# Optimization experiments

Hardware: AMD Instinct MI355X
Metric: run time of the kernel (lower is better)

Reference implementation:

```python
import jax, jax.numpy as jnp
import numpy as np

B, L, R, E, H = 256, 196, 1024, 1024, 512  # batch, regions, rnn_size, input_encoding, att_hid


def _lstm_cell(x, h, c, Wih, Whh, bih, bhh):
    # PyTorch LSTMCell gate order: i, f, g, o
    gates = x @ Wih.T + bih + h @ Whh.T + bhh  # [B, 4R]
    i, f, g, o = jnp.split(gates, 4, axis=1)
    i, f, o = jax.nn.sigmoid(i), jax.nn.sigmoid(f), jax.nn.sigmoid(o)
    g = jnp.tanh(g)
    c_new = f * c + i * g
    h_new = o * jnp.tanh(c_new)
    return h_new, c_new


def _attention(h, att_feats, p_att, mask, Wh, bh, Wa, ba):
    att_h = h @ Wh.T + bh                       # [B, H]
    dot = jnp.tanh(p_att + att_h[:, None, :])   # [B, L, H]
    scores = jnp.einsum('blh,h->bl', dot, Wa) + ba  # [B, L]
    w = jax.nn.softmax(scores, axis=1)
    w = w * mask
    w = w / (jnp.sum(w, axis=1, keepdims=True) + 1e-10)
    return jnp.einsum('bl,bld->bd', w, att_feats)  # [B, R]


def setup_inputs() -> dict:
    key = jax.random.key(0)
    ks = jax.random.split(key, 32)
    s = 0.05
    inp = {
        'xt': jax.random.normal(ks[0], (B, E), jnp.float32),
        'fc_feats': jax.random.normal(ks[1], (B, 3 * R), jnp.float32),
        'att_feats': jax.random.normal(ks[2], (B, L, R), jnp.float32),
        'p_att_feats': jax.random.normal(ks[3], (B, L, H), jnp.float32),
        'att_masks': jnp.ones((B, L), jnp.float32),
        'att_feats1': jax.random.normal(ks[4], (B, L, R), jnp.float32),
        'p_att_feats1': jax.random.normal(ks[5], (B, L, H), jnp.float32),
        'att_masks1': jnp.ones((B, L), jnp.float32),
        'state_h': jax.random.normal(ks[6], (3, B, R), jnp.float32),
        'state_c': jax.random.normal(ks[7], (3, B, R), jnp.float32),
        # att_lstm0 / att_lstm: input dim E + 2R; lang_lstm: 3R
        'Wih0': jax.random.normal(ks[8], (4 * R, E + 2 * R), jnp.float32) * s,
        'Whh0': jax.random.normal(ks[9], (4 * R, R), jnp.float32) * s,
        'bih0': jnp.zeros((4 * R,), jnp.float32),
        'bhh0': jnp.zeros((4 * R,), jnp.float32),
        'Wih1': jax.random.normal(ks[10], (4 * R, E + 2 * R), jnp.float32) * s,
        'Whh1': jax.random.normal(ks[11], (4 * R, R), jnp.float32) * s,
        'bih1': jnp.zeros((4 * R,), jnp.float32),
        'bhh1': jnp.zeros((4 * R,), jnp.float32),
        'WihL': jax.random.normal(ks[12], (4 * R, 3 * R), jnp.float32) * s,
        'WhhL': jax.random.normal(ks[13], (4 * R, R), jnp.float32) * s,
        'bihL': jnp.zeros((4 * R,), jnp.float32),
        'bhhL': jnp.zeros((4 * R,), jnp.float32),
        # attention0 / attention / attention1 params (h2att + alpha_net)
        'a0_Wh': jax.random.normal(ks[14], (H, R), jnp.float32) * s,
        'a0_bh': jnp.zeros((H,), jnp.float32),
        'a0_Wa': jax.random.normal(ks[15], (H,), jnp.float32) * s,
        'a0_ba': jnp.zeros((), jnp.float32),
        'a_Wh': jax.random.normal(ks[16], (H, R), jnp.float32) * s,
        'a_bh': jnp.zeros((H,), jnp.float32),
        'a_Wa': jax.random.normal(ks[17], (H,), jnp.float32) * s,
        'a_ba': jnp.zeros((), jnp.float32),
        'a1_Wh': jax.random.normal(ks[18], (H, R), jnp.float32) * s,
        'a1_bh': jnp.zeros((H,), jnp.float32),
        'a1_Wa': jax.random.normal(ks[19], (H,), jnp.float32) * s,
        'a1_ba': jnp.zeros((), jnp.float32),
    }
    return inp


def reference(xt, fc_feats, att_feats, p_att_feats, att_masks,
              att_feats1, p_att_feats1, att_masks1, state_h, state_c,
              Wih0, Whh0, bih0, bhh0, Wih1, Whh1, bih1, bhh1,
              WihL, WhhL, bihL, bhhL,
              a0_Wh, a0_bh, a0_Wa, a0_ba,
              a_Wh, a_bh, a_Wa, a_ba,
              a1_Wh, a1_bh, a1_Wa, a1_ba):
    prev_h = state_h[-1]                       # h_lang from previous step
    fc_ori = fc_feats[:, :R]                   # only the first slice is used

    # layer 0: att_lstm0 + attention0 over (att_feats1, p_att_feats1)
    x0 = jnp.concatenate([prev_h, fc_ori, xt], axis=1)
    h_att0, c_att0 = _lstm_cell(x0, state_h[0], state_c[0], Wih0, Whh0, bih0, bhh0)
    att0 = _attention(h_att0, att_feats1, p_att_feats1, att_masks1, a0_Wh, a0_bh, a0_Wa, a0_ba)

    # layer 1: att_lstm + two attentions
    x1 = jnp.concatenate([prev_h, att0, xt], axis=1)
    h_att, c_att = _lstm_cell(x1, state_h[1], state_c[1], Wih1, Whh1, bih1, bhh1)
    att = _attention(h_att, att_feats, p_att_feats, att_masks, a_Wh, a_bh, a_Wa, a_ba)
    att1 = _attention(h_att, att_feats1, p_att_feats1, att_masks1, a1_Wh, a1_bh, a1_Wa, a1_ba)

    # layer 2: lang_lstm
    xL = jnp.concatenate([att, att1, h_att], axis=1)
    h_lang, c_lang = _lstm_cell(xL, state_h[2], state_c[2], WihL, WhhL, bihL, bhhL)

    output = h_lang  # dropout is identity in eval mode
    new_h = jnp.stack([h_att0, h_att, h_lang])
    new_c = jnp.stack([c_att0, c_att, c_lang])
    return output, new_h, new_c
```

## Files before the change

kernel.cpp:

```cpp
#include <hip/hip_runtime.h>
#include <math.h>

#define B_   256
#define L_   196
#define R_   1024
#define E_   1024
#define H_   512
#define G4R  4096
#define DIN  3072

__device__ __forceinline__ float sigmoidf_(float x) {
    return 1.0f / (1.0f + __expf(-x));
}
__device__ __forceinline__ float tanhf_(float x) {
    float ax = fabsf(x);
    float t  = __expf(-2.0f * ax);
    float r  = (1.0f - t) / (1.0f + t);
    return copysignf(r, x);
}

__global__ __launch_bounds__(256) void gemm2_bias(
    const float* __restrict__ A1, const float* __restrict__ W1, int K1,
    const float* __restrict__ A2, const float* __restrict__ W2, int K2,
    const float* __restrict__ bias1, const float* __restrict__ bias2,
    float* __restrict__ C, int N)
{
    __shared__ float As[16][64];
    __shared__ float Ws[16][64];
    const int t  = threadIdx.x;
    const int tx = t & 15, ty = t >> 4;
    const int mBase = blockIdx.x * 64;
    const int nBase = blockIdx.y * 64;
    const int lr = t >> 2;
    const int lk = (t & 3) * 4;

    float acc[4][4];
#pragma unroll
    for (int i = 0; i < 4; i++)
#pragma unroll
        for (int j = 0; j < 4; j++) acc[i][j] = 0.0f;

    for (int seg = 0; seg < 2; ++seg) {
        const int K = seg ? K2 : K1;
        if (K == 0) continue;
        const float* A = seg ? A2 : A1;
        const float* W = seg ? W2 : W1;
        const float* aPtr = A + (size_t)(mBase + lr) * K + lk;
        const float* wPtr = W + (size_t)(nBase + lr) * K + lk;

        float4 av = *(const float4*)(aPtr);
        float4 wv = *(const float4*)(wPtr);

        for (int k0 = 0; k0 < K; k0 += 16) {
            float4 avn, wvn;
            if (k0 + 16 < K) {
                avn = *(const float4*)(aPtr + k0 + 16);
                wvn = *(const float4*)(wPtr + k0 + 16);
            } else { avn = av; wvn = wv; }

            __syncthreads();
            As[lk + 0][lr] = av.x; As[lk + 1][lr] = av.y;
            As[lk + 2][lr] = av.z; As[lk + 3][lr] = av.w;
            Ws[lk + 0][lr] = wv.x; Ws[lk + 1][lr] = wv.y;
            Ws[lk + 2][lr] = wv.z; Ws[lk + 3][lr] = wv.w;
            __syncthreads();

#pragma unroll
            for (int k = 0; k < 16; k++) {
                float4 a = *(const float4*)&As[k][ty * 4];
                float4 b = *(const float4*)&Ws[k][tx * 4];
                acc[0][0] += a.x * b.x; acc[0][1] += a.x * b.y;
                acc[0][2] += a.x * b.z; acc[0][3] += a.x * b.w;
                acc[1][0] += a.y * b.x; acc[1][1] += a.y * b.y;
                acc[1][2] += a.y * b.z; acc[1][3] += a.y * b.w;
                acc[2][0] += a.z * b.x; acc[2][1] += a.z * b.y;
                acc[2][2] += a.z * b.z; acc[2][3] += a.z * b.w;
                acc[3][0] += a.w * b.x; acc[3][1] += a.w * b.y;
                acc[3][2] += a.w * b.z; acc[3][3] += a.w * b.w;
            }
            av = avn; wv = wvn;
        }
    }

#pragma unroll
    for (int i = 0; i < 4; i++) {
        int m = mBase + ty * 4 + i;
#pragma unroll
        for (int j = 0; j < 4; j++) {
            int n = nBase + tx * 4 + j;
            float v = acc[i][j] + bias1[n];
            if (bias2) v += bias2[n];
            C[(size_t)m * N + n] = v;
        }
    }
}

__global__ __launch_bounds__(256) void lstm_cell(
    const float* __restrict__ gates, const float* __restrict__ c_in,
    float* __restrict__ h_out, float* __restrict__ c_out,
    float* __restrict__ h_out2)
{
    int e = blockIdx.x * 256 + threadIdx.x;
    int b = e >> 10;
    int j = e & 1023;
    const float* g = gates + (size_t)b * G4R;
    float i_ = sigmoidf_(g[j]);
    float f_ = sigmoidf_(g[j + 1024]);
    float gg = tanhf_(g[j + 2048]);
    float o_ = sigmoidf_(g[j + 3072]);
    float c  = f_ * c_in[e] + i_ * gg;
    float h  = o_ * tanhf_(c);
    c_out[e] = c;
    h_out[e] = h;
    if (h_out2) h_out2[e] = h;
}

__global__ __launch_bounds__(256) void concat3_1024(
    float* __restrict__ dst,
    const float* __restrict__ s0, int ld0,
    const float* __restrict__ s1, int ld1,
    const float* __restrict__ s2, int ld2)
{
    int e = blockIdx.x * 256 + threadIdx.x;
    int b = e / 3072;
    int c = e - b * 3072;
    int which = c >> 10, off = c & 1023;
    const float* s = (which == 0) ? s0 : (which == 1) ? s1 : s2;
    int ld = (which == 0) ? ld0 : (which == 1) ? ld1 : ld2;
    dst[e] = s[(size_t)b * ld + off];
}

__global__ __launch_bounds__(64) void attn_scores(
    const float* __restrict__ p_att,
    const float* __restrict__ att_h,
    const float* __restrict__ Wa,
    const float* __restrict__ ba,
    float* __restrict__ scores)
{
    int l = blockIdx.x;
    int b = blockIdx.y;
    int lane = threadIdx.x;
    const float* p  = p_att + ((size_t)b * L_ + l) * H_;
    const float* ah = att_h + (size_t)b * H_;
    float sum = 0.0f;
#pragma unroll
    for (int i = 0; i < H_ / 64; i++) {
        int h = lane + i * 64;
        sum += tanhf_(p[h] + ah[h]) * Wa[h];
    }
    for (int off = 32; off; off >>= 1) sum += __shfl_down(sum, off);
    if (lane == 0) scores[(size_t)b * L_ + l] = sum + ba[0];
}

__global__ __launch_bounds__(256) void attn_softmax(
    const float* __restrict__ scores, const float* __restrict__ mask,
    float* __restrict__ w)
{
    int b = blockIdx.x;
    int t = threadIdx.x;
    __shared__ float red[256];
    float v = (t < L_) ? scores[(size_t)b * L_ + t] : -1e30f;
    red[t] = v; __syncthreads();
    for (int s = 128; s; s >>= 1) {
        if (t < s) red[t] = fmaxf(red[t], red[t + s]);
        __syncthreads();
    }
    float mx = red[0]; __syncthreads();
    float e = (t < L_) ? __expf(v - mx) : 0.0f;
    red[t] = e; __syncthreads();
    for (int s = 128; s; s >>= 1) {
        if (t < s) red[t] += red[t + s];
        __syncthreads();
    }
    float denom = red[0]; __syncthreads();
    float wm = (t < L_) ? (e / denom) * mask[(size_t)b * L_ + t] : 0.0f;
    red[t] = wm; __syncthreads();
    for (int s = 128; s; s >>= 1) {
        if (t < s) red[t] += red[t + s];
        __syncthreads();
    }
    float denom2 = red[0] + 1e-10f;
    if (t < L_) w[(size_t)b * L_ + t] = wm / denom2;
}

__global__ __launch_bounds__(256) void attn_wsum(
    const float* __restrict__ w,
    const float* __restrict__ feats,
    float* __restrict__ out)
{
    int b = blockIdx.y;
    int r = blockIdx.x * 256 + threadIdx.x;
    __shared__ float ws[L_];
    for (int i = threadIdx.x; i < L_; i += 256)
        ws[i] = w[(size_t)b * L_ + i];
    __syncthreads();
    const float* f = feats + (size_t)b * L_ * R_ + r;
    float a0 = 0, a1 = 0, a2 = 0, a3 = 0;
    for (int l = 0; l < L_; l += 4) {
        a0 += ws[l + 0] * f[(size_t)(l + 0) * R_];
        a1 += ws[l + 1] * f[(size_t)(l + 1) * R_];
        a2 += ws[l + 2] * f[(size_t)(l + 2) * R_];
        a3 += ws[l + 3] * f[(size_t)(l + 3) * R_];
    }
    out[(size_t)b * R_ + r] = a0 + a1 + a2 + a3;
}

extern "C" void kernel_launch(void* const* d_in, const int* in_sizes, int n_in,
                              void* d_out, int out_size, void* d_ws, size_t ws_size,
                              hipStream_t stream)
{
    const float* xt         = (const float*)d_in[0];
    const float* fc_feats   = (const float*)d_in[1];
    const float* att_feats  = (const float*)d_in[2];
    const float* p_att      = (const float*)d_in[3];
    const float* mask       = (const float*)d_in[4];
    const float* att_feats1 = (const float*)d_in[5];
    const float* p_att1     = (const float*)d_in[6];
    const float* mask1      = (const float*)d_in[7];
    const float* state_h    = (const float*)d_in[8];
    const float* state_c    = (const float*)d_in[9];
    const float* Wih0 = (const float*)d_in[10];
    const float* Whh0 = (const float*)d_in[11];
    const float* bih0 = (const float*)d_in[12];
    const float* bhh0 = (const float*)d_in[13];
    const float* Wih1 = (const float*)d_in[14];
    const float* Whh1 = (const float*)d_in[15];
    const float* bih1 = (const float*)d_in[16];
    const float* bhh1 = (const float*)d_in[17];
    const float* WihL = (const float*)d_in[18];
    const float* WhhL = (const float*)d_in[19];
    const float* bihL = (const float*)d_in[20];
    const float* bhhL = (const float*)d_in[21];
    const float* a0_Wh = (const float*)d_in[22];
    const float* a0_bh = (const float*)d_in[23];
    const float* a0_Wa = (const float*)d_in[24];
    const float* a0_ba = (const float*)d_in[25];
    const float* a_Wh  = (const float*)d_in[26];
    const float* a_bh  = (const float*)d_in[27];
    const float* a_Wa  = (const float*)d_in[28];
    const float* a_ba  = (const float*)d_in[29];
    const float* a1_Wh = (const float*)d_in[30];
    const float* a1_bh = (const float*)d_in[31];
    const float* a1_Wa = (const float*)d_in[32];
    const float* a1_ba = (const float*)d_in[33];

    const size_t BR = (size_t)B_ * R_;
    float* out   = (float*)d_out;
    float* h0    = out + 1 * BR;
    float* h1    = out + 2 * BR;
    float* h2    = out + 3 * BR;
    float* c0    = out + 4 * BR;
    float* c1    = out + 5 * BR;
    float* c2    = out + 6 * BR;

    float* xbuf  = (float*)d_ws;
    float* gates = xbuf + (size_t)B_ * DIN;
    float* atth  = gates + (size_t)B_ * G4R;
    float* sc    = atth + (size_t)B_ * H_;
    float* att0  = sc + (size_t)B_ * L_;
    float* attA  = att0 + BR;
    float* attB  = attA + BR;

    const float* prev_h = state_h + 2 * BR;

    dim3 gG(B_ / 64, G4R / 64);
    dim3 gA(B_ / 64, H_ / 64);
    dim3 gS(L_, B_);
    dim3 gW(R_ / 256, B_);

    concat3_1024<<<(B_ * DIN) / 256, 256, 0, stream>>>(xbuf, prev_h, R_, fc_feats, 3 * R_, xt, E_);
    gemm2_bias<<<gG, 256, 0, stream>>>(xbuf, Wih0, DIN, state_h, Whh0, R_, bih0, bhh0, gates, G4R);
    lstm_cell<<<(B_ * R_) / 256, 256, 0, stream>>>(gates, state_c, h0, c0, nullptr);

    gemm2_bias<<<gA, 256, 0, stream>>>(h0, a0_Wh, R_, nullptr, nullptr, 0, a0_bh, nullptr, atth, H_);
    attn_scores<<<gS, 64, 0, stream>>>(p_att1, atth, a0_Wa, a0_ba, sc);
    attn_softmax<<<B_, 256, 0, stream>>>(sc, mask1, sc);
    attn_wsum<<<gW, 256, 0, stream>>>(sc, att_feats1, att0);

    concat3_1024<<<(B_ * DIN) / 256, 256, 0, stream>>>(xbuf, prev_h, R_, att0, R_, xt, E_);
    gemm2_bias<<<gG, 256, 0, stream>>>(xbuf, Wih1, DIN, state_h + BR, Whh1, R_, bih1, bhh1, gates, G4R);
    lstm_cell<<<(B_ * R_) / 256, 256, 0, stream>>>(gates, state_c + BR, h1, c1, nullptr);

    gemm2_bias<<<gA, 256, 0, stream>>>(h1, a_Wh, R_, nullptr, nullptr, 0, a_bh, nullptr, atth, H_);
    attn_scores<<<gS, 64, 0, stream>>>(p_att, atth, a_Wa, a_ba, sc);
    attn_softmax<<<B_, 256, 0, stream>>>(sc, mask, sc);
    attn_wsum<<<gW, 256, 0, stream>>>(sc, att_feats, attA);

    gemm2_bias<<<gA, 256, 0, stream>>>(h1, a1_Wh, R_, nullptr, nullptr, 0, a1_bh, nullptr, atth, H_);
    attn_scores<<<gS, 64, 0, stream>>>(p_att1, atth, a1_Wa, a1_ba, sc);
    attn_softmax<<<B_, 256, 0, stream>>>(sc, mask1, sc);
    attn_wsum<<<gW, 256, 0, stream>>>(sc, att_feats1, attB);

    concat3_1024<<<(B_ * DIN) / 256, 256, 0, stream>>>(xbuf, attA, R_, attB, R_, h1, R_);
    gemm2_bias<<<gG, 256, 0, stream>>>(xbuf, WihL, DIN, state_h + 2 * BR, WhhL, R_, bihL, bhhL, gates, G4R);
    lstm_cell<<<(B_ * R_) / 256, 256, 0, stream>>>(gates, state_c + 2 * BR, h2, c2, out);
}
```

Before: 1.458 ms.

## Replace FP32 SIMT GEMM with split-bf16 MFMA GEMM for LSTM and attention projections

Replaces the scalar FP32 tiled GEMM with an MFMA-based kernel. Each fp32 operand is split into high and low bf16 halves, and three bf16 MFMAs (hi*hi, hi*lo, lo*hi) approximate fp32 accuracy. The goal is to move the dominant gate GEMMs onto the matrix cores instead of the vector ALUs. The small attention-projection GEMMs now use 32x32 tiles, launching more blocks. The cost is extra conversion work during shared-memory staging, slightly lower precision than true fp32, and no global-load prefetch across k-steps.

Measured after the change: 1.219 ms. -16.4%, faster.

```diff
diff --git a/kernel.cpp b/kernel.cpp
--- a/kernel.cpp
+++ b/kernel.cpp
@@ -9,6 +9,10 @@
 #define G4R  4096
 #define DIN  3072
 
+typedef short v4s __attribute__((ext_vector_type(4)));
+typedef short v8s __attribute__((ext_vector_type(8)));
+typedef float v4f __attribute__((ext_vector_type(4)));
+
 __device__ __forceinline__ float sigmoidf_(float x) {
     return 1.0f / (1.0f + __expf(-x));
 }
@@ -19,78 +23,117 @@
     return copysignf(r, x);
 }
 
-__global__ __launch_bounds__(256) void gemm2_bias(
-    const float* __restrict__ A1, const float* __restrict__ W1, int K1,
-    const float* __restrict__ A2, const float* __restrict__ W2, int K2,
+__device__ __forceinline__ void split2(float x, short& hi, short& lo) {
+    unsigned u = __float_as_uint(x);
+    hi = (short)(u >> 16);
+    float r = x - __uint_as_float(u & 0xFFFF0000u);
+    lo = (short)(__float_as_uint(r) >> 16);
+}
+
+template<int MT, int NT>
+__global__ __launch_bounds__(256) void gemm_mfma(
+    const float* __restrict__ A1, const float* __restrict__ W1, int K1, int lda1,
+    const float* __restrict__ A2, const float* __restrict__ W2, int K2, int lda2,
     const float* __restrict__ bias1, const float* __restrict__ bias2,
     float* __restrict__ C, int N)
 {
-    __shared__ float As[16][64];
-    __shared__ float Ws[16][64];
-    const int t  = threadIdx.x;
-    const int tx = t & 15, ty = t >> 4;
-    const int mBase = blockIdx.x * 64;
-    const int nBase = blockIdx.y * 64;
-    const int lr = t >> 2;
-    const int lk = (t & 3) * 4;
-
-    float acc[4][4];
-#pragma unroll
-    for (int i = 0; i < 4; i++)
-#pragma unroll
-        for (int j = 0; j < 4; j++) acc[i][j] = 0.0f;
+    constexpr int FM  = MT / 32;
+    constexpr int FN  = NT / 32;
+    constexpr int ACH = (MT * 32) / 1024;
+    constexpr int WCH = (NT * 32) / 1024;
+
+    __shared__ alignas(16) short Ahi[MT][40];
+    __shared__ alignas(16) short Alo[MT][40];
+    __shared__ alignas(16) short Whi[NT][40];
+    __shared__ alignas(16) short Wlo[NT][40];
+
+    const int t     = threadIdx.x;
+    const int lane  = t & 63;
+    const int wave  = t >> 6;
+    const int waveM = wave & 1;
+    const int waveN = wave >> 1;
+    const int l16   = lane & 15;
+    const int quad  = lane >> 4;
+    const int mBase = blockIdx.x * MT;
+    const int nBase = blockIdx.y * NT;
+
+    v4f acc[FM][FN] = {};
 
     for (int seg = 0; seg < 2; ++seg) {
         const int K = seg ? K2 : K1;
         if (K == 0) continue;
-        const float* A = seg ? A2 : A1;
-        const float* W = seg ? W2 : W1;
-        const float* aPtr = A + (size_t)(mBase + lr) * K + lk;
-        const float* wPtr = W + (size_t)(nBase + lr) * K + lk;
-
-        float4 av = *(const float4*)(aPtr);
-        float4 wv = *(const float4*)(wPtr);
-
-        for (int k0 = 0; k0 < K; k0 += 16) {
-            float4 avn, wvn;
-            if (k0 + 16 < K) {
-                avn = *(const float4*)(aPtr + k0 + 16);
-                wvn = *(const float4*)(wPtr + k0 + 16);
-            } else { avn = av; wvn = wv; }
-
+        const float* Ag  = seg ? A2 : A1;
+        const float* Wg  = seg ? W2 : W1;
+        const int    lda = seg ? lda2 : lda1;
+
+        for (int k0 = 0; k0 < K; k0 += 32) {
             __syncthreads();
-            As[lk + 0][lr] = av.x; As[lk + 1][lr] = av.y;
-            As[lk + 2][lr] = av.z; As[lk + 3][lr] = av.w;
-            Ws[lk + 0][lr] = wv.x; Ws[lk + 1][lr] = wv.y;
-            Ws[lk + 2][lr] = wv.z; Ws[lk + 3][lr] = wv.w;
+            #pragma unroll
+            for (int c = 0; c < ACH; ++c) {
+                int flat = t * 4 + c * 1024;
+                int row  = flat >> 5, k = flat & 31;
+                float4 v = *(const float4*)(Ag + (size_t)(mBase + row) * lda + k0 + k);
+                short h0, h1, h2, h3, l0, l1, l2, l3;
+                split2(v.x, h0, l0); split2(v.y, h1, l1);
+                split2(v.z, h2, l2); split2(v.w, h3, l3);
+                v4s hv = { h0, h1, h2, h3 };
+                v4s lv = { l0, l1, l2, l3 };
+                *(v4s*)&Ahi[row][k] = hv;
+                *(v4s*)&Alo[row][k] = lv;
+            }
+            #pragma unroll
+            for (int c = 0; c < WCH; ++c) {
+                int flat = t * 4 + c * 1024;
+                int row  = flat >> 5, k = flat & 31;
+                float4 v = *(const float4*)(Wg + (size_t)(nBase + row) * K + k0 + k);
+                short h0, h1, h2, h3, l0, l1, l2, l3;
+                split2(v.x, h0, l0); split2(v.y, h1, l1);
+                split2(v.z, h2, l2); split2(v.w, h3, l3);
+                v4s hv = { h0, h1, h2, h3 };
+                v4s lv = { l0, l1, l2, l3 };
+                *(v4s*)&Whi[row][k] = hv;
+                *(v4s*)&Wlo[row][k] = lv;
+            }
             __syncthreads();
 
-#pragma unroll
-            for (int k = 0; k < 16; k++) {
-                float4 a = *(const float4*)&As[k][ty * 4];
-                float4 b = *(const float4*)&Ws[k][tx * 4];
-                acc[0][0] += a.x * b.x; acc[0][1] += a.x * b.y;
-                acc[0][2] += a.x * b.z; acc[0][3] += a.x * b.w;
-                acc[1][0] += a.y * b.x; acc[1][1] += a.y * b.y;
-                acc[1][2] += a.y * b.z; acc[1][3] += a.y * b.w;
-                acc[2][0] += a.z * b.x; acc[2][1] += a.z * b.y;
-                acc[2][2] += a.z * b.z; acc[2][3] += a.z * b.w;
-                acc[3][0] += a.w * b.x; acc[3][1] += a.w * b.y;
-                acc[3][2] += a.w * b.z; acc[3][3] += a.w * b.w;
+            v8s ah[FM], al[FM], wh[FN], wl[FN];
+            #pragma unroll
+            for (int fi = 0; fi < FM; ++fi) {
+                int r = waveM * (MT / 2) + fi * 16 + l16;
+                ah[fi] = *(const v8s*)&Ahi[r][quad * 8];
+                al[fi] = *(const v8s*)&Alo[r][quad * 8];
             }
-            av = avn; wv = wvn;
+            #pragma unroll
+            for (int fj = 0; fj < FN; ++fj) {
+                int r = waveN * (NT / 2) + fj * 16 + l16;
+                wh[fj] = *(const v8s*)&Whi[r][quad * 8];
+                wl[fj] = *(const v8s*)&Wlo[r][quad * 8];
+            }
+
+            #pragma unroll
+            for (int fi = 0; fi < FM; ++fi)
+                #pragma unroll
+                for (int fj = 0; fj < FN; ++fj) {
+                    acc[fi][fj] = __builtin_amdgcn_mfma_f32_16x16x32_bf16(
+                        al[fi], wh[fj], acc[fi][fj], 0, 0, 0);
+                    acc[fi][fj] = __builtin_amdgcn_mfma_f32_16x16x32_bf16(
+                        ah[fi], wl[fj], acc[fi][fj], 0, 0, 0);
+                    acc[fi][fj] = __builtin_amdgcn_mfma_f32_16x16x32_bf16(
+                        ah[fi], wh[fj], acc[fi][fj], 0, 0, 0);
+                }
         }
     }
 
-#pragma unroll
-    for (int i = 0; i < 4; i++) {
-        int m = mBase + ty * 4 + i;
-#pragma unroll
-        for (int j = 0; j < 4; j++) {
-            int n = nBase + tx * 4 + j;
-            float v = acc[i][j] + bias1[n];
-            if (bias2) v += bias2[n];
-            C[(size_t)m * N + n] = v;
+    #pragma unroll
+    for (int fj = 0; fj < FN; ++fj) {
+        int n = nBase + waveN * (NT / 2) + fj * 16 + l16;
+        float bb = bias1[n] + (bias2 ? bias2[n] : 0.0f);
+        #pragma unroll
+        for (int fi = 0; fi < FM; ++fi) {
+            int m0 = mBase + waveM * (MT / 2) + fi * 16 + quad * 4;
+            #pragma unroll
+            for (int r = 0; r < 4; ++r)
+                C[(size_t)(m0 + r) * N + n] = acc[fi][fj][r] + bb;
         }
     }
 }
@@ -264,34 +307,46 @@
     const float* prev_h = state_h + 2 * BR;
 
     dim3 gG(B_ / 64, G4R / 64);
-    dim3 gA(B_ / 64, H_ / 64);
+    dim3 gA(B_ / 32, H_ / 32);
     dim3 gS(L_, B_);
     dim3 gW(R_ / 256, B_);
 
     concat3_1024<<<(B_ * DIN) / 256, 256, 0, stream>>>(xbuf, prev_h, R_, fc_feats, 3 * R_, xt, E_);
-    gemm2_bias<<<gG, 256, 0, stream>>>(xbuf, Wih0, DIN, state_h, Whh0, R_, bih0, bhh0, gates, G4R);
+    gemm_mfma<64, 64><<<gG, 256, 0, stream>>>(xbuf, Wih0, DIN, DIN,
+                                              state_h, Whh0, R_, R_,
+                                              bih0, bhh0, gates, G4R);
     lstm_cell<<<(B_ * R_) / 256, 256, 0, stream>>>(gates, state_c, h0, c0, nullptr);
 
-    gemm2_bias<<<gA, 256, 0, stream>>>(h0, a0_Wh, R_, nullptr, nullptr, 0, a0_bh, nullptr, atth, H_);
+    gemm_mfma<32, 32><<<gA, 256, 0, stream>>>(h0, a0_Wh, R_, R_,
+                                              nullptr, nullptr, 0, 0,
+                                              a0_bh, nullptr, atth, H_);
     attn_scores<<<gS, 64, 0, stream>>>(p_att1, atth, a0_Wa, a0_ba, sc);
     attn_softmax<<<B_, 256, 0, stream>>>(sc, mask1, sc);
     attn_wsum<<<gW, 256, 0, stream>>>(sc, att_feats1, att0);
 
     concat3_1024<<<(B_ * DIN) / 256, 256, 0, stream>>>(xbuf, prev_h, R_, att0, R_, xt, E_);
-    gemm2_bias<<<gG, 256, 0, stream>>>(xbuf, Wih1, DIN, state_h + BR, Whh1, R_, bih1, bhh1, gates, G4R);
+    gemm_mfma<64, 64><<<gG, 256, 0, stream>>>(xbuf, Wih1, DIN, DIN,
+                                              state_h + BR, Whh1, R_, R_,
+                                              bih1, bhh1, gates, G4R);
     lstm_cell<<<(B_ * R_) / 256, 256, 0, stream>>>(gates, state_c + BR, h1, c1, nullptr);
 
-    gemm2_bias<<<gA, 256, 0, stream>>>(h1, a_Wh, R_, nullptr, nullptr, 0, a_bh, nullptr, atth, H_);
+    gemm_mfma<32, 32><<<gA, 256, 0, stream>>>(h1, a_Wh, R_, R_,
+                                              nullptr, nullptr, 0, 0,
+                                              a_bh, nullptr, atth, H_);
     attn_scores<<<gS, 64, 0, stream>>>(p_att, atth, a_Wa, a_ba, sc);
     attn_softmax<<<B_, 256, 0, stream>>>(sc, mask, sc);
     attn_wsum<<<gW, 256, 0, stream>>>(sc, att_feats, attA);
 
-    gemm2_bias<<<gA, 256, 0, stream>>>(h1, a1_Wh, R_, nullptr, nullptr, 0, a1_bh, nullptr, atth, H_);
+    gemm_mfma<32, 32><<<gA, 256, 0, stream>>>(h1, a1_Wh, R_, R_,
+                                              nullptr, nullptr, 0, 0,
+                                              a1_bh, nullptr, atth, H_);
     attn_scores<<<gS, 64, 0, stream>>>(p_att1, atth, a1_Wa, a1_ba, sc);
     attn_softmax<<<B_, 256, 0, stream>>>(sc, mask1, sc);
     attn_wsum<<<gW, 256, 0, stream>>>(sc, att_feats1, attB);
 
     concat3_1024<<<(B_ * DIN) / 256, 256, 0, stream>>>(xbuf, attA, R_, attB, R_, h1, R_);
-    gemm2_bias<<<gG, 256, 0, stream>>>(xbuf, WihL, DIN, state_h + 2 * BR, WhhL, R_, bihL, bhhL, gates, G4R);
+    gemm_mfma<64, 64><<<gG, 256, 0, stream>>>(xbuf, WihL, DIN, DIN,
+                                              state_h + 2 * BR, WhhL, R_, R_,
+                                              bihL, bhhL, gates, G4R);
     lstm_cell<<<(B_ * R_) / 256, 256, 0, stream>>>(gates, state_c + 2 * BR, h2, c2, out);
 }
```
